# Kernel tuning notes

Hardware: AMD Instinct MI355X
Metric: run time of the kernel (lower is better)

The kernel has to match this reference:

```python
import jax, jax.numpy as jnp
import numpy as np

H = 1024
W = 1024
N = 4194304


def setup_inputs() -> dict:
    key = jax.random.key(0)
    k1, k2 = jax.random.split(key)
    inputs = jax.random.uniform(k1, (N, 2), dtype=jnp.float32)  # query points (x, v)
    grid = jax.random.normal(k2, (H, W), dtype=jnp.float32)     # 2-D lookup table f(x, v)
    bounds = jnp.array([[0.0, 1.0], [0.0, 1.0]], dtype=jnp.float32)  # [[x_lo,x_hi],[v_lo,v_hi]]
    return {"inputs": inputs, "grid": grid, "bounds": bounds}


def _axis_coords(q, size):
    # TF _interpolate_bilinear: floor clamped to [0, size-2], alpha clamped to [0, 1]
    fl = jnp.clip(jnp.floor(q), 0.0, size - 2.0)
    alpha = jnp.clip(q - fl, 0.0, 1.0)
    return fl.astype(jnp.int32), alpha


def reference(inputs, grid, bounds):
    h = jnp.float32(grid.shape[0])
    w = jnp.float32(grid.shape[1])
    # normalized fractional indices (ij indexing: dim0 = x-row, dim1 = v-col)
    qy = (h - 1.0) * (inputs[:, 0] - bounds[0, 0]) / (bounds[0, 1] - bounds[0, 0])
    qx = (w - 1.0) * (inputs[:, 1] - bounds[1, 0]) / (bounds[1, 1] - bounds[1, 0])
    y0, ay = _axis_coords(qy, grid.shape[0])
    x0, ax = _axis_coords(qx, grid.shape[1])
    # 4-point gather + bilinear blend
    tl = grid[y0, x0]
    tr = grid[y0, x0 + 1]
    bl = grid[y0 + 1, x0]
    br = grid[y0 + 1, x0 + 1]
    top = tl + (tr - tl) * ax
    bot = bl + (br - bl) * ax
    out = top + (bot - top) * ay
    return out[None, :, None]  # [1, N, 1] to match _interpolate_bilinear output
```

## Files before the change

kernel.cpp:

```cpp
#include <hip/hip_runtime.h>


#define GRID_H 1024
#define GRID_W 1024

typedef float floatx4 __attribute__((ext_vector_type(4)));
typedef float floatx2 __attribute__((ext_vector_type(2)));
typedef unsigned int uintx2 __attribute__((ext_vector_type(2)));
typedef unsigned int uintx4 __attribute__((ext_vector_type(4)));

__device__ __forceinline__ unsigned int f32_to_bf16_rne(float f) {
    unsigned int u = __builtin_bit_cast(unsigned int, f);
    u += 0x7fffu + ((u >> 16) & 1u);
    return u >> 16;
}

__global__ __launch_bounds__(256) void buildPair_kernel(
    const float* __restrict__ grid,
    unsigned int* __restrict__ pair,
    int n_groups)
{
    int g = blockIdx.x * blockDim.x + threadIdx.x;
    if (g >= n_groups) return;
    int idx = g * 4;
    int y = idx >> 10;
    int x = idx & (GRID_W - 1);
    const floatx4* r0 = (const floatx4*)(grid + (y << 10) + x);
    const floatx4* r1 = (const floatx4*)(grid + ((y + 1) << 10) + x);
    floatx4 t = *r0;
    floatx4 b = *r1;
    uintx4 o;
    o.x = f32_to_bf16_rne(t.x) | (f32_to_bf16_rne(b.x) << 16);
    o.y = f32_to_bf16_rne(t.y) | (f32_to_bf16_rne(b.y) << 16);
    o.z = f32_to_bf16_rne(t.z) | (f32_to_bf16_rne(b.z) << 16);
    o.w = f32_to_bf16_rne(t.w) | (f32_to_bf16_rne(b.w) << 16);
    *(uintx4*)(pair + idx) = o;
}

__global__ __launch_bounds__(256) void interpPair_kernel(
    const float* __restrict__ in,
    const unsigned int* __restrict__ pair,
    const float* __restrict__ bounds,
    float* __restrict__ out,
    int n_pts)
{
    const int H = GRID_H, W = GRID_W;
    const float x_lo = bounds[0];
    const float x_hi = bounds[1];
    const float v_lo = bounds[2];
    const float v_hi = bounds[3];
    const float sy = (float)(H - 1) / (x_hi - x_lo);
    const float sx = (float)(W - 1) / (v_hi - v_lo);

    const int t = blockIdx.x * blockDim.x + threadIdx.x;
    const int base = t * 8;
    if (base >= n_pts) return;

    float xs[8], vs[8], res[8];

    if (base + 7 < n_pts) {
        const floatx4* in4 = (const floatx4*)in;
#pragma unroll
        for (int q = 0; q < 4; ++q) {
            floatx4 p = __builtin_nontemporal_load(&in4[4 * t + q]);
            xs[2 * q + 0] = p.x; vs[2 * q + 0] = p.y;
            xs[2 * q + 1] = p.z; vs[2 * q + 1] = p.w;
        }
    } else {
#pragma unroll
        for (int k = 0; k < 8; ++k) {
            int p = base + k < n_pts ? base + k : n_pts - 1;
            xs[k] = in[2 * p + 0];
            vs[k] = in[2 * p + 1];
        }
    }

    float ays[8], axs[8];
    int qidx[8];
#pragma unroll
    for (int k = 0; k < 8; ++k) {
        float qy = (xs[k] - x_lo) * sy;
        float qx = (vs[k] - v_lo) * sx;
        float fy = fminf(fmaxf(floorf(qy), 0.0f), (float)(H - 2));
        float fx = fminf(fmaxf(floorf(qx), 0.0f), (float)(W - 2));
        ays[k] = fminf(fmaxf(qy - fy, 0.0f), 1.0f);
        axs[k] = fminf(fmaxf(qx - fx, 0.0f), 1.0f);
        qidx[k] = ((int)fy << 10) + (int)fx;
    }

    uintx2 c[8];
#pragma unroll
    for (int k = 0; k < 8; ++k)
        c[k] = *(const uintx2*)(pair + qidx[k]);

#pragma unroll
    for (int k = 0; k < 8; ++k) {
        float tl = __builtin_bit_cast(float, c[k].x << 16);
        float bl = __builtin_bit_cast(float, c[k].x & 0xffff0000u);
        float tr = __builtin_bit_cast(float, c[k].y << 16);
        float br = __builtin_bit_cast(float, c[k].y & 0xffff0000u);
        float top = tl + (tr - tl) * axs[k];
        float bot = bl + (br - bl) * axs[k];
        res[k] = top + (bot - top) * ays[k];
    }

    if (base + 7 < n_pts) {
        floatx4* out4 = (floatx4*)out;
#pragma unroll
        for (int q = 0; q < 2; ++q) {
            floatx4 o;
            o.x = res[4 * q + 0]; o.y = res[4 * q + 1];
            o.z = res[4 * q + 2]; o.w = res[4 * q + 3];
            __builtin_nontemporal_store(o, &out4[2 * t + q]);
        }
    } else {
#pragma unroll
        for (int k = 0; k < 8; ++k)
            if (base + k < n_pts) out[base + k] = res[k];
    }
}

__global__ __launch_bounds__(256) void interpRaw_kernel(
    const float* __restrict__ in, const float* __restrict__ grid,
    const float* __restrict__ bounds, float* __restrict__ out, int n_pts)
{
    const int H = GRID_H, W = GRID_W;
    const float x_lo = bounds[0], x_hi = bounds[1];
    const float v_lo = bounds[2], v_hi = bounds[3];
    const float sy = (float)(H - 1) / (x_hi - x_lo);
    const float sx = (float)(W - 1) / (v_hi - v_lo);
    const int t = blockIdx.x * blockDim.x + threadIdx.x;
    const int base = t * 4;
    if (base >= n_pts) return;
    float xs[4], vs[4], res[4];
#pragma unroll
    for (int k = 0; k < 4; ++k) {
        int p = base + k < n_pts ? base + k : n_pts - 1;
        xs[k] = in[2 * p + 0];
        vs[k] = in[2 * p + 1];
    }
    float ays[4], axs[4];
    const floatx2 *gt[4], *gb[4];
#pragma unroll
    for (int k = 0; k < 4; ++k) {
        float qy = (xs[k] - x_lo) * sy;
        float qx = (vs[k] - v_lo) * sx;
        float fy = fminf(fmaxf(floorf(qy), 0.0f), (float)(H - 2));
        float fx = fminf(fmaxf(floorf(qx), 0.0f), (float)(W - 2));
        ays[k] = fminf(fmaxf(qy - fy, 0.0f), 1.0f);
        axs[k] = fminf(fmaxf(qx - fx, 0.0f), 1.0f);
        const float* g = grid + ((int)fy << 10) + (int)fx;
        gt[k] = (const floatx2*)g;
        gb[k] = (const floatx2*)(g + W);
    }
    floatx2 t2[4], b2[4];
#pragma unroll
    for (int k = 0; k < 4; ++k) { t2[k] = *gt[k]; b2[k] = *gb[k]; }
#pragma unroll
    for (int k = 0; k < 4; ++k) {
        float top = t2[k].x + (t2[k].y - t2[k].x) * axs[k];
        float bot = b2[k].x + (b2[k].y - b2[k].x) * axs[k];
        res[k] = top + (bot - top) * ays[k];
    }
#pragma unroll
    for (int k = 0; k < 4; ++k)
        if (base + k < n_pts) out[base + k] = res[k];
}

extern "C" void kernel_launch(void* const* d_in, const int* in_sizes, int n_in,
                              void* d_out, int out_size, void* d_ws, size_t ws_size,
                              hipStream_t stream) {
    const float* in     = (const float*)d_in[0];
    const float* grid   = (const float*)d_in[1];
    const float* bounds = (const float*)d_in[2];
    float* out = (float*)d_out;

    const int n_pts = in_sizes[0] / 2;
    const int n_entries = (GRID_H - 1) * GRID_W;
    const size_t pair_bytes = (size_t)n_entries * 4;

    if (ws_size >= pair_bytes) {
        unsigned int* pair = (unsigned int*)d_ws;
        const int n_groups = n_entries / 4;
        buildPair_kernel<<<(n_groups + 255) / 256, 256, 0, stream>>>(grid, pair, n_groups);
        const int n_threads = (n_pts + 7) / 8;
        interpPair_kernel<<<(n_threads + 255) / 256, 256, 0, stream>>>(
            in, pair, bounds, out, n_pts);
    } else {
        const int n_threads = (n_pts + 3) / 4;
        interpRaw_kernel<<<(n_threads + 255) / 256, 256, 0, stream>>>(
            in, grid, bounds, out, n_pts);
    }
}
```

Measured before the change: 114.3 us.

## Drop bf16 pair-table prebuild and gather directly from fp32 grid

Removes the preprocessing kernel that packed vertically adjacent grid rows into a bf16 pair table. The interpolation kernel now gathers two floatx2 values (top and bottom rows) straight from the fp32 grid, 8 points per thread. Addressing uses a single base pointer offset by half a row so both loads can share one address with immediate offsets. This saves a kernel launch and the 4MB table write, but each point now needs two gather loads and the 4MB fp32 grid has a larger cache footprint than the table.

```diff
diff --git a/kernel.cpp b/kernel.cpp
--- a/kernel.cpp
+++ b/kernel.cpp
@@ -6,40 +6,10 @@
 
 typedef float floatx4 __attribute__((ext_vector_type(4)));
 typedef float floatx2 __attribute__((ext_vector_type(2)));
-typedef unsigned int uintx2 __attribute__((ext_vector_type(2)));
-typedef unsigned int uintx4 __attribute__((ext_vector_type(4)));
 
-__device__ __forceinline__ unsigned int f32_to_bf16_rne(float f) {
-    unsigned int u = __builtin_bit_cast(unsigned int, f);
-    u += 0x7fffu + ((u >> 16) & 1u);
-    return u >> 16;
-}
-
-__global__ __launch_bounds__(256) void buildPair_kernel(
+__global__ __launch_bounds__(256) void interpRaw8_kernel(
+    const float* __restrict__ in,
     const float* __restrict__ grid,
-    unsigned int* __restrict__ pair,
-    int n_groups)
-{
-    int g = blockIdx.x * blockDim.x + threadIdx.x;
-    if (g >= n_groups) return;
-    int idx = g * 4;
-    int y = idx >> 10;
-    int x = idx & (GRID_W - 1);
-    const floatx4* r0 = (const floatx4*)(grid + (y << 10) + x);
-    const floatx4* r1 = (const floatx4*)(grid + ((y + 1) << 10) + x);
-    floatx4 t = *r0;
-    floatx4 b = *r1;
-    uintx4 o;
-    o.x = f32_to_bf16_rne(t.x) | (f32_to_bf16_rne(b.x) << 16);
-    o.y = f32_to_bf16_rne(t.y) | (f32_to_bf16_rne(b.y) << 16);
-    o.z = f32_to_bf16_rne(t.z) | (f32_to_bf16_rne(b.z) << 16);
-    o.w = f32_to_bf16_rne(t.w) | (f32_to_bf16_rne(b.w) << 16);
-    *(uintx4*)(pair + idx) = o;
-}
-
-__global__ __launch_bounds__(256) void interpPair_kernel(
-    const float* __restrict__ in,
-    const unsigned int* __restrict__ pair,
     const float* __restrict__ bounds,
     float* __restrict__ out,
     int n_pts)
@@ -76,7 +46,7 @@
     }
 
     float ays[8], axs[8];
-    int qidx[8];
+    const float* gp[8];
 #pragma unroll
     for (int k = 0; k < 8; ++k) {
         float qy = (xs[k] - x_lo) * sy;
@@ -85,22 +55,19 @@
         float fx = fminf(fmaxf(floorf(qx), 0.0f), (float)(W - 2));
         ays[k] = fminf(fmaxf(qy - fy, 0.0f), 1.0f);
         axs[k] = fminf(fmaxf(qx - fx, 0.0f), 1.0f);
-        qidx[k] = ((int)fy << 10) + (int)fx;
+        gp[k] = grid + (((int)fy << 10) + (int)fx + 512);
     }
 
-    uintx2 c[8];
+    floatx2 t2[8], b2[8];
 #pragma unroll
-    for (int k = 0; k < 8; ++k)
-        c[k] = *(const uintx2*)(pair + qidx[k]);
+    for (int k = 0; k < 8; ++k) t2[k] = *(const floatx2*)(gp[k] - 512);
+#pragma unroll
+    for (int k = 0; k < 8; ++k) b2[k] = *(const floatx2*)(gp[k] + 512);
 
 #pragma unroll
     for (int k = 0; k < 8; ++k) {
-        float tl = __builtin_bit_cast(float, c[k].x << 16);
-        float bl = __builtin_bit_cast(float, c[k].x & 0xffff0000u);
-        float tr = __builtin_bit_cast(float, c[k].y << 16);
-        float br = __builtin_bit_cast(float, c[k].y & 0xffff0000u);
-        float top = tl + (tr - tl) * axs[k];
-        float bot = bl + (br - bl) * axs[k];
+        float top = t2[k].x + (t2[k].y - t2[k].x) * axs[k];
+        float bot = b2[k].x + (b2[k].y - b2[k].x) * axs[k];
         res[k] = top + (bot - top) * ays[k];
     }
 
@@ -120,53 +87,6 @@
     }
 }
 
-__global__ __launch_bounds__(256) void interpRaw_kernel(
-    const float* __restrict__ in, const float* __restrict__ grid,
-    const float* __restrict__ bounds, float* __restrict__ out, int n_pts)
-{
-    const int H = GRID_H, W = GRID_W;
-    const float x_lo = bounds[0], x_hi = bounds[1];
-    const float v_lo = bounds[2], v_hi = bounds[3];
-    const float sy = (float)(H - 1) / (x_hi - x_lo);
-    const float sx = (float)(W - 1) / (v_hi - v_lo);
-    const int t = blockIdx.x * blockDim.x + threadIdx.x;
-    const int base = t * 4;
-    if (base >= n_pts) return;
-    float xs[4], vs[4], res[4];
-#pragma unroll
-    for (int k = 0; k < 4; ++k) {
-        int p = base + k < n_pts ? base + k : n_pts - 1;
-        xs[k] = in[2 * p + 0];
-        vs[k] = in[2 * p + 1];
-    }
-    float ays[4], axs[4];
-    const floatx2 *gt[4], *gb[4];
-#pragma unroll
-    for (int k = 0; k < 4; ++k) {
-        float qy = (xs[k] - x_lo) * sy;
-        float qx = (vs[k] - v_lo) * sx;
-        float fy = fminf(fmaxf(floorf(qy), 0.0f), (float)(H - 2));
-        float fx = fminf(fmaxf(floorf(qx), 0.0f), (float)(W - 2));
-        ays[k] = fminf(fmaxf(qy - fy, 0.0f), 1.0f);
-        axs[k] = fminf(fmaxf(qx - fx, 0.0f), 1.0f);
-        const float* g = grid + ((int)fy << 10) + (int)fx;
-        gt[k] = (const floatx2*)g;
-        gb[k] = (const floatx2*)(g + W);
-    }
-    floatx2 t2[4], b2[4];
-#pragma unroll
-    for (int k = 0; k < 4; ++k) { t2[k] = *gt[k]; b2[k] = *gb[k]; }
-#pragma unroll
-    for (int k = 0; k < 4; ++k) {
-        float top = t2[k].x + (t2[k].y - t2[k].x) * axs[k];
-        float bot = b2[k].x + (b2[k].y - b2[k].x) * axs[k];
-        res[k] = top + (bot - top) * ays[k];
-    }
-#pragma unroll
-    for (int k = 0; k < 4; ++k)
-        if (base + k < n_pts) out[base + k] = res[k];
-}
-
 extern "C" void kernel_launch(void* const* d_in, const int* in_sizes, int n_in,
                               void* d_out, int out_size, void* d_ws, size_t ws_size,
                               hipStream_t stream) {
@@ -176,19 +96,8 @@
     float* out = (float*)d_out;
 
     const int n_pts = in_sizes[0] / 2;
-    const int n_entries = (GRID_H - 1) * GRID_W;
-    const size_t pair_bytes = (size_t)n_entries * 4;
-
-    if (ws_size >= pair_bytes) {
-        unsigned int* pair = (unsigned int*)d_ws;
-        const int n_groups = n_entries / 4;
-        buildPair_kernel<<<(n_groups + 255) / 256, 256, 0, stream>>>(grid, pair, n_groups);
-        const int n_threads = (n_pts + 7) / 8;
-        interpPair_kernel<<<(n_threads + 255) / 256, 256, 0, stream>>>(
-            in, pair, bounds, out, n_pts);
-    } else {
-        const int n_threads = (n_pts + 3) / 4;
-        interpRaw_kernel<<<(n_threads + 255) / 256, 256, 0, stream>>>(
-            in, grid, bounds, out, n_pts);
-    }
+    const int n_threads = (n_pts + 7) / 8;
+    (void)d_ws; (void)ws_size;
+    interpRaw8_kernel<<<(n_threads + 255) / 256, 256, 0, stream>>>(
+        in, grid, bounds, out, n_pts);
 }
```

New measurement: 128.8 us. +12.7%, slower.
